# Performance work log

Measured on AMD Instinct MI355X. Metric: run time of the kernel, lower is better.

Reference implementation:

```python
import jax, jax.numpy as jnp
import numpy as np

SHAPES = ((100, 100), (50, 50), (25, 25))  # (H_l, W_l) per level
D, HEADS, HD, L, P = 256, 8, 32, 3, 4


def setup_inputs() -> dict:
    key = jax.random.key(0)
    ks = jax.random.split(key, 12)
    B = 2
    Nq = sum(h * w for h, w in SHAPES)  # 13125
    inp = {
        "query": jax.random.normal(ks[0], (B, Nq, D), jnp.float32),
        "reference_points": jax.random.uniform(ks[1], (B, Nq, L, 2), jnp.float32),
        "value0": jax.random.normal(ks[2], (B, SHAPES[0][0] * SHAPES[0][1], D), jnp.float32),
        "value1": jax.random.normal(ks[3], (B, SHAPES[1][0] * SHAPES[1][1], D), jnp.float32),
        "value2": jax.random.normal(ks[4], (B, SHAPES[2][0] * SHAPES[2][1], D), jnp.float32),
        "W_val": jax.random.normal(ks[5], (D, D), jnp.float32) * 0.05,
        "b_val": jnp.zeros((D,), jnp.float32),
        "W_off": jax.random.normal(ks[6], (D, HEADS * L * P * 2), jnp.float32) * 0.01,
        "b_off": jax.random.normal(ks[7], (HEADS * L * P * 2,), jnp.float32) * 2.0,
        "W_attn": jax.random.normal(ks[8], (D, HEADS * L * P), jnp.float32) * 0.02,
        "b_attn": jnp.zeros((HEADS * L * P,), jnp.float32),
        "W_out": jax.random.normal(ks[9], (D, D), jnp.float32) * 0.05,
        "b_out": jnp.zeros((D,), jnp.float32),
    }
    return inp


def _bilinear_sample(v, Hl, Wl, loc):
    """v: (B, heads, Hl*Wl, hd); loc: (B, Nq, heads, P, 2) normalized coords in [0,1].
    Matches torch F.grid_sample(mode='bilinear', padding_mode='zeros', align_corners=False)
    applied to grid = 2*loc - 1. Returns (B, Nq, heads, P, hd)."""
    B, heads, _, hd = v.shape
    Nq, Pn = loc.shape[1], loc.shape[3]
    # align_corners=False: pixel = ((g+1)*size - 1)/2 with g = 2*loc-1  ->  loc*size - 0.5
    x = loc[..., 0] * Wl - 0.5
    y = loc[..., 1] * Hl - 0.5
    x0 = jnp.floor(x)
    y0 = jnp.floor(y)
    wx1 = x - x0
    wy1 = y - y0
    out = jnp.zeros((B, Nq, heads, Pn, hd), v.dtype)
    for xi, wx in ((x0, 1.0 - wx1), (x0 + 1.0, wx1)):
        for yi, wy in ((y0, 1.0 - wy1), (y0 + 1.0, wy1)):
            inb = (xi >= 0) & (xi < Wl) & (yi >= 0) & (yi < Hl)
            idx = (jnp.clip(yi, 0, Hl - 1) * Wl + jnp.clip(xi, 0, Wl - 1)).astype(jnp.int32)
            idx_t = idx.transpose(0, 2, 1, 3).reshape(B, heads, Nq * Pn)  # (B,H,Nq*P)
            g = jnp.take_along_axis(v, idx_t[..., None], axis=2)  # (B,H,Nq*P,hd)
            g = g.reshape(B, heads, Nq, Pn, hd).transpose(0, 2, 1, 3, 4)
            w = (wx * wy * inb).astype(v.dtype)  # (B,Nq,heads,P)
            out = out + g * w[..., None]
    return out


def _forward(query, reference_points, values, W_val, b_val, W_off, b_off, W_attn, b_attn, W_out, b_out):
    B, Nq, _ = query.shape
    offs = (query @ W_off + b_off).reshape(B, Nq, HEADS, L, P, 2)
    attn = jax.nn.softmax((query @ W_attn + b_attn).reshape(B, Nq, HEADS, L * P), axis=-1)
    attn = attn.reshape(B, Nq, HEADS, L, P)
    out = jnp.zeros((B, Nq, HEADS, HD), query.dtype)
    for lvl, (Hl, Wl) in enumerate(SHAPES):
        # project values, split heads: (B, heads, H*W, hd)
        v = (values[lvl] @ W_val + b_val).reshape(B, Hl * Wl, HEADS, HD).transpose(0, 2, 1, 3)
        norm = jnp.array([Wl, Hl], query.dtype)
        loc = reference_points[:, :, lvl][:, :, None, None, :] + offs[:, :, :, lvl] / norm  # (B,Nq,heads,P,2)
        sampled = _bilinear_sample(v, Hl, Wl, loc)  # (B,Nq,heads,P,hd)
        out = out + jnp.einsum('bnhp,bnhpd->bnhd', attn[:, :, :, lvl], sampled)
    out = out.reshape(B, Nq, D)
    return out @ W_out + b_out  # dropout is identity at eval


def reference(query, reference_points, value0, value1, value2, W_val, b_val, W_off, b_off, W_attn, b_attn, W_out, b_out):
    return _forward(query, reference_points, (value0, value1, value2), W_val, b_val, W_off, b_off, W_attn, b_attn, W_out, b_out)
```

## Files before the change

kernel.cpp:

```cpp
#include <hip/hip_runtime.h>
#include <hip/hip_bf16.h>
#include <math.h>

#define BATCH 2
#define NQ    13125
#define MQ    26250
#define DM    256
#define NH    8
#define HDIM  32
#define NL    3
#define NP    4
#define NTOK  13125

typedef __attribute__((ext_vector_type(8))) short bf16x8;
typedef __attribute__((ext_vector_type(4))) float f32x4;

__device__ __forceinline__ short f2bf(float f) {
    unsigned u = __float_as_uint(f);
    unsigned r = (u + 0x7FFFu + ((u >> 16) & 1u)) >> 16;
    return (short)r;
}
__device__ __forceinline__ float bf2f(unsigned short u) {
    return __uint_as_float((unsigned)u << 16);
}

__global__ __launch_bounds__(256) void wprep_kernel(const float* __restrict__ Wv,
                                                    const float* __restrict__ Wo,
                                                    const float* __restrict__ Wa,
                                                    const float* __restrict__ Wu,
                                                    short* __restrict__ Wt)
{
    const int w = blockIdx.y;
    const int Ns[4]   = {256, 192, 96, 256};
    const int Offs[4] = {0, 256 * 256, 256 * 256 + 192 * 256, 256 * 256 + 192 * 256 + 96 * 256};
    const float* W = (w == 0) ? Wv : ((w == 1) ? Wo : ((w == 2) ? Wa : Wu));
    const int N = Ns[w];
    const int flat = blockIdx.x * 256 + threadIdx.x;
    const int n = flat >> 8, k = flat & 255;
    if (n < N) Wt[Offs[w] + n * 256 + k] = f2bf(W[k * N + n]);
}

__global__ __launch_bounds__(256) void cvt_kernel(const float* __restrict__ q,
                                                  const float* __restrict__ v0,
                                                  const float* __restrict__ v1,
                                                  const float* __restrict__ v2,
                                                  short* __restrict__ qb,
                                                  short* __restrict__ v0b,
                                                  short* __restrict__ v1b,
                                                  short* __restrict__ v2b)
{
    const int t = blockIdx.y;
    const int sz4[4] = {MQ * 64, 2 * 10000 * 64, 2 * 2500 * 64, 2 * 625 * 64};
    const float* src = (t == 0) ? q : ((t == 1) ? v0 : ((t == 2) ? v1 : v2));
    short* dst = (t == 0) ? qb : ((t == 1) ? v0b : ((t == 2) ? v1b : v2b));
    const int i = blockIdx.x * 256 + threadIdx.x;
    if (i < sz4[t]) {
        float4 v = ((const float4*)src)[i];
        short4 o;
        o.x = f2bf(v.x); o.y = f2bf(v.y); o.z = f2bf(v.z); o.w = f2bf(v.w);
        ((short4*)dst)[i] = o;
    }
}

template<int EPI>
__device__ __forceinline__ void gemm_body(const short* __restrict__ A,
                                          const short* __restrict__ Wt,
                                          const float* __restrict__ bias0,
                                          const float* __restrict__ bias1,
                                          void* __restrict__ C0,
                                          void* __restrict__ C1,
                                          int M, int N, int m0, int n0)
{
    __shared__ short As[128][40];
    __shared__ short Bs[64][40];

    const int tid  = threadIdx.x;
    const int lane = tid & 63;
    const int wave = tid >> 6;
    const int wm   = wave * 32;
    const int ml   = lane & 15;
    const int kq   = lane >> 4;

    const int srow = tid >> 2;
    const int skp  = (tid & 3) * 8;

    f32x4 acc[2][4] = {};

    for (int k0 = 0; k0 < 256; k0 += 32) {
#pragma unroll
        for (int rr = 0; rr < 2; ++rr) {
            const int row = srow + rr * 64;
            bf16x8 t = {};
            if (m0 + row < M) t = *(const bf16x8*)(A + (size_t)(m0 + row) * 256 + k0 + skp);
            *(bf16x8*)&As[row][skp] = t;
        }
        {
            bf16x8 t = {};
            if (n0 + srow < N) t = *(const bf16x8*)(Wt + (size_t)(n0 + srow) * 256 + k0 + skp);
            *(bf16x8*)&Bs[srow][skp] = t;
        }
        __syncthreads();

        bf16x8 af[2], bfr[4];
#pragma unroll
        for (int ti = 0; ti < 2; ++ti) af[ti] = *(const bf16x8*)&As[wm + ti * 16 + ml][kq * 8];
#pragma unroll
        for (int tj = 0; tj < 4; ++tj) bfr[tj] = *(const bf16x8*)&Bs[tj * 16 + ml][kq * 8];
#pragma unroll
        for (int ti = 0; ti < 2; ++ti)
#pragma unroll
            for (int tj = 0; tj < 4; ++tj)
                acc[ti][tj] = __builtin_amdgcn_mfma_f32_16x16x32_bf16(af[ti], bfr[tj], acc[ti][tj], 0, 0, 0);

        __syncthreads();
    }

#pragma unroll
    for (int ti = 0; ti < 2; ++ti) {
#pragma unroll
        for (int tj = 0; tj < 4; ++tj) {
#pragma unroll
            for (int r = 0; r < 4; ++r) {
                const int gm = m0 + wm + ti * 16 + kq * 4 + r;
                const int gn = n0 + tj * 16 + ml;
                if (gm >= M || gn >= N) continue;
                if (EPI == 0) {
                    ((float*)C0)[(size_t)gm * N + gn] = acc[ti][tj][r] + bias0[gn];
                } else if (EPI == 1) {
                    ((short*)C0)[(size_t)gm * N + gn] = f2bf(acc[ti][tj][r] + bias0[gn]);
                } else {
                    if (gn < 192) ((float*)C0)[(size_t)gm * 192 + gn] = acc[ti][tj][r] + bias0[gn];
                    else          ((float*)C1)[(size_t)gm * 96 + gn - 192] = acc[ti][tj][r] + bias1[gn - 192];
                }
            }
        }
    }
}

__global__ __launch_bounds__(256) void qgemm_fused_kernel(const short* __restrict__ A,
                                                          const short* __restrict__ Wt,
                                                          const float* __restrict__ b_off,
                                                          const float* __restrict__ b_attn,
                                                          float* __restrict__ offs,
                                                          float* __restrict__ lgts)
{
    const int m0 = blockIdx.y * 128;
    const int n0 = blockIdx.x * 64;
    gemm_body<2>(A, Wt, b_off, b_attn, offs, lgts, MQ, 288, m0, n0);
}

__global__ __launch_bounds__(256) void ogemm_kernel(const short* __restrict__ A,
                                                    const short* __restrict__ Wt,
                                                    const float* __restrict__ bias,
                                                    float* __restrict__ C)
{
    const int m0 = blockIdx.y * 128;
    const int n0 = blockIdx.x * 64;
    gemm_body<0>(A, Wt, bias, nullptr, C, nullptr, MQ, DM, m0, n0);
}

__global__ __launch_bounds__(256) void vproj_kernel(const short* __restrict__ v0b,
                                                    const short* __restrict__ v1b,
                                                    const short* __restrict__ v2b,
                                                    const short* __restrict__ Wt,
                                                    const float* __restrict__ bias,
                                                    short* __restrict__ vws)
{
    const int z = blockIdx.z;
    const int b = z / 3, l = z % 3;
    const int Ms[3]   = {10000, 2500, 625};
    const int Offs[3] = {0, 10000, 12500};
    const short* Asel = (l == 0) ? v0b : ((l == 1) ? v1b : v2b);
    const int M = Ms[l];
    const short* A = Asel + (size_t)b * M * DM;
    short* C = vws + ((size_t)b * NTOK + Offs[l]) * DM;
    const int m0 = blockIdx.y * 128;
    const int n0 = blockIdx.x * 64;
    if (m0 >= M) return;
    gemm_body<1>(A, Wt, bias, nullptr, C, nullptr, M, DM, m0, n0);
}

__global__ __launch_bounds__(256) void sample_kernel(const short* __restrict__ vws,
                                                     const float* __restrict__ offs,
                                                     const float* __restrict__ logits,
                                                     const float* __restrict__ refp,
                                                     short* __restrict__ mid)
{
    const int q0  = blockIdx.x * 4;
    const int tid = threadIdx.x;

    __shared__ float  s_lg[4][96];
    __shared__ float  s_ref[4][6];
    __shared__ float  s_stat[4][NH][2];
    __shared__ float4 s_w[4][96];
    __shared__ int4   s_i[4][96];

    for (int idx = tid; idx < 384; idx += 256) {
        const int qq = idx / 96, s = idx % 96;
        const int q = q0 + qq;
        if (q < MQ) s_lg[qq][s] = logits[(size_t)q * 96 + s];
    }
    if (tid < 24) {
        const int qq = tid / 6, j = tid % 6;
        const int q = q0 + qq;
        if (q < MQ) s_ref[qq][j] = refp[(size_t)q * 6 + j];
    }
    __syncthreads();

    if (tid < 32) {
        const int qq = tid >> 3, h = tid & 7;
        if (q0 + qq < MQ) {
            float mx = -1e30f;
#pragma unroll
            for (int i = 0; i < 12; ++i) mx = fmaxf(mx, s_lg[qq][h * 12 + i]);
            float ssum = 0.f;
#pragma unroll
            for (int i = 0; i < 12; ++i) ssum += expf(s_lg[qq][h * 12 + i] - mx);
            s_stat[qq][h][0] = mx;
            s_stat[qq][h][1] = 1.f / ssum;
        }
    }
    __syncthreads();

    for (int idx = tid; idx < 384; idx += 256) {
        const int qq = idx / 96, s = idx % 96;
        const int q  = q0 + qq;
        if (q >= MQ) continue;
        const int b  = q / NQ;
        const int h  = s / 12, i = s % 12;
        const int l  = i >> 2, p = i & 3;

        const int Hs[3] = {100, 50, 25};
        const int Wz[3] = {100, 50, 25};
        const int Lo[3] = {0, 10000, 12500};
        const int Wl = Wz[l], Hl = Hs[l];
        const float fW = (float)Wl, fH = (float)Hl;

        const float aw = expf(s_lg[qq][s] - s_stat[qq][h][0]) * s_stat[qq][h][1];

        const int oi = (((h * NL) + l) * NP + p) * 2;
        const float2 offp = *(const float2*)(offs + (size_t)q * 192 + oi);
        const float rx = s_ref[qq][l * 2 + 0];
        const float ry = s_ref[qq][l * 2 + 1];

        const float x = (rx + offp.x / fW) * fW - 0.5f;
        const float y = (ry + offp.y / fH) * fH - 0.5f;
        const float x0f = floorf(x), y0f = floorf(y);
        const int   x0 = (int)x0f,  y0 = (int)y0f;
        const float wx1 = x - x0f, wy1 = y - y0f;
        const float wx0 = 1.f - wx1, wy0 = 1.f - wy1;

        const bool xin0 = (x0 >= 0) && (x0 < Wl);
        const bool xin1 = (x0 + 1 >= 0) && (x0 + 1 < Wl);
        const bool yin0 = (y0 >= 0) && (y0 < Hl);
        const bool yin1 = (y0 + 1 >= 0) && (y0 + 1 < Hl);

        const int cx0 = min(max(x0, 0), Wl - 1);
        const int cx1 = min(max(x0 + 1, 0), Wl - 1);
        const int cy0 = min(max(y0, 0), Hl - 1);
        const int cy1 = min(max(y0 + 1, 0), Hl - 1);

        const int base = b * NTOK + Lo[l];
        int4 idxv;
        idxv.x = base + cy0 * Wl + cx0;
        idxv.y = base + cy0 * Wl + cx1;
        idxv.z = base + cy1 * Wl + cx0;
        idxv.w = base + cy1 * Wl + cx1;

        float4 w;
        w.x = (xin0 && yin0) ? aw * wx0 * wy0 : 0.f;
        w.y = (xin1 && yin0) ? aw * wx1 * wy0 : 0.f;
        w.z = (xin0 && yin1) ? aw * wx0 * wy1 : 0.f;
        w.w = (xin1 && yin1) ? aw * wx1 * wy1 : 0.f;

        s_w[qq][s] = w;
        s_i[qq][s] = idxv;
    }
    __syncthreads();

    {
        const int qq = tid >> 6;
        const int q  = q0 + qq;
        if (q < MQ) {
            const int r  = tid & 63;
            const int h  = r >> 3;
            const int c4 = (r & 7) * 4;
            const int ch = h * HDIM + c4;

            float a0 = 0.f, a1 = 0.f, a2 = 0.f, a3 = 0.f;
#pragma unroll
            for (int s = 0; s < 12; ++s) {
                const float4 w  = s_w[qq][h * 12 + s];
                const int4   id = s_i[qq][h * 12 + s];
                const ushort4 u0 = *(const ushort4*)(vws + (size_t)id.x * DM + ch);
                const ushort4 u1 = *(const ushort4*)(vws + (size_t)id.y * DM + ch);
                const ushort4 u2 = *(const ushort4*)(vws + (size_t)id.z * DM + ch);
                const ushort4 u3 = *(const ushort4*)(vws + (size_t)id.w * DM + ch);
                a0 += w.x * bf2f(u0.x) + w.y * bf2f(u1.x) + w.z * bf2f(u2.x) + w.w * bf2f(u3.x);
                a1 += w.x * bf2f(u0.y) + w.y * bf2f(u1.y) + w.z * bf2f(u2.y) + w.w * bf2f(u3.y);
                a2 += w.x * bf2f(u0.z) + w.y * bf2f(u1.z) + w.z * bf2f(u2.z) + w.w * bf2f(u3.z);
                a3 += w.x * bf2f(u0.w) + w.y * bf2f(u1.w) + w.z * bf2f(u2.w) + w.w * bf2f(u3.w);
            }
            short4 o;
            o.x = f2bf(a0); o.y = f2bf(a1); o.z = f2bf(a2); o.w = f2bf(a3);
            *(short4*)(mid + (size_t)q * DM + ch) = o;
        }
    }
}

extern "C" void kernel_launch(void* const* d_in, const int* in_sizes, int n_in,
                              void* d_out, int out_size, void* d_ws, size_t ws_size,
                              hipStream_t stream)
{
    const float* query  = (const float*)d_in[0];
    const float* refp   = (const float*)d_in[1];
    const float* v0     = (const float*)d_in[2];
    const float* v1     = (const float*)d_in[3];
    const float* v2     = (const float*)d_in[4];
    const float* W_val  = (const float*)d_in[5];
    const float* b_val  = (const float*)d_in[6];
    const float* W_off  = (const float*)d_in[7];
    const float* b_off  = (const float*)d_in[8];
    const float* W_attn = (const float*)d_in[9];
    const float* b_attn = (const float*)d_in[10];
    const float* W_out  = (const float*)d_in[11];
    const float* b_out  = (const float*)d_in[12];
    float* out = (float*)d_out;

    float* ws   = (float*)d_ws;
    float* offs = ws;
    float* lgts = offs + (size_t)MQ * 192;
    short* vws  = (short*)(lgts + (size_t)MQ * 96);
    short* mid  = vws + (size_t)BATCH * NTOK * DM;
    short* qbf  = mid + (size_t)MQ * DM;
    short* v0b  = qbf + (size_t)MQ * DM;
    short* v1b  = v0b + (size_t)2 * 10000 * DM;
    short* v2b  = v1b + (size_t)2 * 2500 * DM;
    short* Wt   = v2b + (size_t)2 * 625 * DM;
    short* Wt_val  = Wt;
    short* Wt_off  = Wt_val + 256 * 256;
    short* Wt_out  = Wt_off + 288 * 256;

    {
        dim3 grid(256, 4);
        wprep_kernel<<<grid, 256, 0, stream>>>(W_val, W_off, W_attn, W_out, Wt);
    }
    {
        dim3 grid((MQ * 64 + 255) / 256, 4);
        cvt_kernel<<<grid, 256, 0, stream>>>(query, v0, v1, v2, qbf, v0b, v1b, v2b);
    }
    {
        dim3 grid(DM / 64, (10000 + 127) / 128, 6);
        vproj_kernel<<<grid, 256, 0, stream>>>(v0b, v1b, v2b, Wt_val, b_val, vws);
    }
    {
        dim3 grid((288 + 63) / 64, (MQ + 127) / 128);
        qgemm_fused_kernel<<<grid, 256, 0, stream>>>(qbf, Wt_off, b_off, b_attn, offs, lgts);
    }
    sample_kernel<<<(MQ + 3) / 4, 256, 0, stream>>>(vws, offs, lgts, refp, mid);
    {
        dim3 grid(DM / 64, (MQ + 127) / 128);
        ogemm_kernel<<<grid, 256, 0, stream>>>(mid, Wt_out, b_out, out);
    }
}
```

Measured before the change: 240.9 us.

## Use 128x128 GEMM tiles with direct global-to-LDS loads and widen sampling gathers

Replaces the 128x64 GEMM with a 128x128 tile kernel. It loads A and B straight into LDS via global_load_lds and uses an XOR-swizzled LDS layout to avoid bank conflicts. Value tensors are converted into one concatenated buffer so the value projection becomes a single GEMM launch, and the offset/attention weight matrix is zero-padded to 384 columns. The sampling kernel moves to 128 threads with 8-wide bf16 gathers and byte offsets precomputed in the index table. Larger tiles cut redundant operand loads and launches, but lower block count, occupancy and padding waste are risks.

```diff
diff --git a/kernel.cpp b/kernel.cpp
--- a/kernel.cpp
+++ b/kernel.cpp
@@ -13,6 +13,7 @@
 #define NTOK  13125
 
 typedef __attribute__((ext_vector_type(8))) short bf16x8;
+typedef __attribute__((ext_vector_type(8))) unsigned short u16x8;
 typedef __attribute__((ext_vector_type(4))) float f32x4;
 
 __device__ __forceinline__ short f2bf(float f) {
@@ -22,6 +23,12 @@
 }
 __device__ __forceinline__ float bf2f(unsigned short u) {
     return __uint_as_float((unsigned)u << 16);
+}
+
+__device__ __forceinline__ void gld_lds16(const short* g, short* l) {
+    __builtin_amdgcn_global_load_lds(
+        (const __attribute__((address_space(1))) unsigned int*)g,
+        (__attribute__((address_space(3))) unsigned int*)l, 16, 0, 0);
 }
 
 __global__ __launch_bounds__(256) void wprep_kernel(const float* __restrict__ Wv,
@@ -31,13 +38,15 @@
                                                     short* __restrict__ Wt)
 {
     const int w = blockIdx.y;
-    const int Ns[4]   = {256, 192, 96, 256};
-    const int Offs[4] = {0, 256 * 256, 256 * 256 + 192 * 256, 256 * 256 + 192 * 256 + 96 * 256};
-    const float* W = (w == 0) ? Wv : ((w == 1) ? Wo : ((w == 2) ? Wa : Wu));
+    const int Ns[5]   = {256, 192, 96, 256, 96};
+    const int Offs[5] = {0, 65536, 114688, 163840, 139264};
     const int N = Ns[w];
     const int flat = blockIdx.x * 256 + threadIdx.x;
     const int n = flat >> 8, k = flat & 255;
-    if (n < N) Wt[Offs[w] + n * 256 + k] = f2bf(W[k * N + n]);
+    if (n >= N) return;
+    if (w == 4) { Wt[139264 + n * 256 + k] = 0; return; }
+    const float* W = (w == 0) ? Wv : ((w == 1) ? Wo : ((w == 2) ? Wa : Wu));
+    Wt[Offs[w] + n * 256 + k] = f2bf(W[k * N + n]);
 }
 
 __global__ __launch_bounds__(256) void cvt_kernel(const float* __restrict__ q,
@@ -45,69 +54,83 @@
                                                   const float* __restrict__ v1,
                                                   const float* __restrict__ v2,
                                                   short* __restrict__ qb,
-                                                  short* __restrict__ v0b,
-                                                  short* __restrict__ v1b,
-                                                  short* __restrict__ v2b)
+                                                  short* __restrict__ vcat)
 {
     const int t = blockIdx.y;
     const int sz4[4] = {MQ * 64, 2 * 10000 * 64, 2 * 2500 * 64, 2 * 625 * 64};
+    const int i = blockIdx.x * 256 + threadIdx.x;
+    if (i >= sz4[t]) return;
+    const int row = i >> 6, c = i & 63;
     const float* src = (t == 0) ? q : ((t == 1) ? v0 : ((t == 2) ? v1 : v2));
-    short* dst = (t == 0) ? qb : ((t == 1) ? v0b : ((t == 2) ? v1b : v2b));
-    const int i = blockIdx.x * 256 + threadIdx.x;
-    if (i < sz4[t]) {
-        float4 v = ((const float4*)src)[i];
-        short4 o;
-        o.x = f2bf(v.x); o.y = f2bf(v.y); o.z = f2bf(v.z); o.w = f2bf(v.w);
-        ((short4*)dst)[i] = o;
-    }
-}
-
-template<int EPI>
-__device__ __forceinline__ void gemm_body(const short* __restrict__ A,
-                                          const short* __restrict__ Wt,
-                                          const float* __restrict__ bias0,
-                                          const float* __restrict__ bias1,
-                                          void* __restrict__ C0,
-                                          void* __restrict__ C1,
-                                          int M, int N, int m0, int n0)
-{
-    __shared__ short As[128][40];
-    __shared__ short Bs[64][40];
+    int orow;
+    short* dst;
+    if (t == 0)      { orow = row;                                        dst = qb; }
+    else if (t == 1) { orow = (row / 10000) * NTOK + (row % 10000);       dst = vcat; }
+    else if (t == 2) { orow = (row / 2500) * NTOK + 10000 + (row % 2500); dst = vcat; }
+    else             { orow = (row / 625) * NTOK + 12500 + (row % 625);   dst = vcat; }
+    float4 v = ((const float4*)src)[i];
+    short4 o;
+    o.x = f2bf(v.x); o.y = f2bf(v.y); o.z = f2bf(v.z); o.w = f2bf(v.w);
+    ((short4*)dst)[orow * 64 + c] = o;
+}
+
+template<int EPI, int NN>
+__global__ __launch_bounds__(256) void gemm128(const short* __restrict__ A,
+                                               const short* __restrict__ Wt,
+                                               const float* __restrict__ bias0,
+                                               const float* __restrict__ bias1,
+                                               void* __restrict__ C0,
+                                               void* __restrict__ C1)
+{
+    __shared__ short As[128 * 32];
+    __shared__ short Bs[128 * 32];
 
     const int tid  = threadIdx.x;
+    const int m0   = blockIdx.y * 128;
+    const int n0   = blockIdx.x * 128;
     const int lane = tid & 63;
     const int wave = tid >> 6;
-    const int wm   = wave * 32;
+    const int wm   = (wave & 1) * 64;
+    const int wn   = (wave >> 1) * 64;
     const int ml   = lane & 15;
     const int kq   = lane >> 4;
 
-    const int srow = tid >> 2;
-    const int skp  = (tid & 3) * 8;
-
-    f32x4 acc[2][4] = {};
+    const int row0 = tid >> 2;
+    const int row1 = row0 + 64;
+    const int kqs  = (tid & 3) ^ ((row0 >> 1) & 3);
+    const short* gA0 = A  + (size_t)(m0 + row0) * 256 + kqs * 8;
+    const short* gA1 = A  + (size_t)(m0 + row1) * 256 + kqs * 8;
+    const short* gB0 = Wt + (size_t)(n0 + row0) * 256 + kqs * 8;
+    const short* gB1 = Wt + (size_t)(n0 + row1) * 256 + kqs * 8;
+    short* lA0 = As + tid * 8;
+    short* lA1 = As + (256 + tid) * 8;
+    short* lB0 = Bs + tid * 8;
+    short* lB1 = Bs + (256 + tid) * 8;
+    const bool a0ok = (m0 + row0) < MQ;
+    const bool a1ok = (m0 + row1) < MQ;
+
+    f32x4 acc[4][4] = {};
 
     for (int k0 = 0; k0 < 256; k0 += 32) {
-#pragma unroll
-        for (int rr = 0; rr < 2; ++rr) {
-            const int row = srow + rr * 64;
-            bf16x8 t = {};
-            if (m0 + row < M) t = *(const bf16x8*)(A + (size_t)(m0 + row) * 256 + k0 + skp);
-            *(bf16x8*)&As[row][skp] = t;
-        }
-        {
-            bf16x8 t = {};
-            if (n0 + srow < N) t = *(const bf16x8*)(Wt + (size_t)(n0 + srow) * 256 + k0 + skp);
-            *(bf16x8*)&Bs[srow][skp] = t;
-        }
+        if (a0ok) gld_lds16(gA0 + k0, lA0);
+        if (a1ok) gld_lds16(gA1 + k0, lA1);
+        gld_lds16(gB0 + k0, lB0);
+        gld_lds16(gB1 + k0, lB1);
         __syncthreads();
 
-        bf16x8 af[2], bfr[4];
-#pragma unroll
-        for (int ti = 0; ti < 2; ++ti) af[ti] = *(const bf16x8*)&As[wm + ti * 16 + ml][kq * 8];
-#pragma unroll
-        for (int tj = 0; tj < 4; ++tj) bfr[tj] = *(const bf16x8*)&Bs[tj * 16 + ml][kq * 8];
-#pragma unroll
-        for (int ti = 0; ti < 2; ++ti)
+        bf16x8 af[4], bfr[4];
+#pragma unroll
+        for (int ti = 0; ti < 4; ++ti) {
+            const int r = wm + ti * 16 + ml;
+            af[ti] = *(const bf16x8*)&As[r * 32 + ((kq ^ ((r >> 1) & 3)) << 3)];
+        }
+#pragma unroll
+        for (int tj = 0; tj < 4; ++tj) {
+            const int r = wn + tj * 16 + ml;
+            bfr[tj] = *(const bf16x8*)&Bs[r * 32 + ((kq ^ ((r >> 1) & 3)) << 3)];
+        }
+#pragma unroll
+        for (int ti = 0; ti < 4; ++ti)
 #pragma unroll
             for (int tj = 0; tj < 4; ++tj)
                 acc[ti][tj] = __builtin_amdgcn_mfma_f32_16x16x32_bf16(af[ti], bfr[tj], acc[ti][tj], 0, 0, 0);
@@ -116,71 +139,29 @@
     }
 
 #pragma unroll
-    for (int ti = 0; ti < 2; ++ti) {
-#pragma unroll
-        for (int tj = 0; tj < 4; ++tj) {
+    for (int tj = 0; tj < 4; ++tj) {
+        const int gn = n0 + wn + tj * 16 + ml;
+#pragma unroll
+        for (int ti = 0; ti < 4; ++ti) {
 #pragma unroll
             for (int r = 0; r < 4; ++r) {
                 const int gm = m0 + wm + ti * 16 + kq * 4 + r;
-                const int gn = n0 + tj * 16 + ml;
-                if (gm >= M || gn >= N) continue;
+                if (gm >= MQ) continue;
+                const float v = acc[ti][tj][r];
                 if (EPI == 0) {
-                    ((float*)C0)[(size_t)gm * N + gn] = acc[ti][tj][r] + bias0[gn];
+                    ((float*)C0)[(size_t)gm * NN + gn] = v + bias0[gn];
                 } else if (EPI == 1) {
-                    ((short*)C0)[(size_t)gm * N + gn] = f2bf(acc[ti][tj][r] + bias0[gn]);
+                    ((short*)C0)[(size_t)gm * NN + gn] = f2bf(v + bias0[gn]);
                 } else {
-                    if (gn < 192) ((float*)C0)[(size_t)gm * 192 + gn] = acc[ti][tj][r] + bias0[gn];
-                    else          ((float*)C1)[(size_t)gm * 96 + gn - 192] = acc[ti][tj][r] + bias1[gn - 192];
+                    if (gn < 192)      ((float*)C0)[(size_t)gm * 192 + gn]        = v + bias0[gn];
+                    else if (gn < 288) ((float*)C1)[(size_t)gm * 96 + (gn - 192)] = v + bias1[gn - 192];
                 }
             }
         }
     }
 }
 
-__global__ __launch_bounds__(256) void qgemm_fused_kernel(const short* __restrict__ A,
-                                                          const short* __restrict__ Wt,
-                                                          const float* __restrict__ b_off,
-                                                          const float* __restrict__ b_attn,
-                                                          float* __restrict__ offs,
-                                                          float* __restrict__ lgts)
-{
-    const int m0 = blockIdx.y * 128;
-    const int n0 = blockIdx.x * 64;
-    gemm_body<2>(A, Wt, b_off, b_attn, offs, lgts, MQ, 288, m0, n0);
-}
-
-__global__ __launch_bounds__(256) void ogemm_kernel(const short* __restrict__ A,
-                                                    const short* __restrict__ Wt,
-                                                    const float* __restrict__ bias,
-                                                    float* __restrict__ C)
-{
-    const int m0 = blockIdx.y * 128;
-    const int n0 = blockIdx.x * 64;
-    gemm_body<0>(A, Wt, bias, nullptr, C, nullptr, MQ, DM, m0, n0);
-}
-
-__global__ __launch_bounds__(256) void vproj_kernel(const short* __restrict__ v0b,
-                                                    const short* __restrict__ v1b,
-                                                    const short* __restrict__ v2b,
-                                                    const short* __restrict__ Wt,
-                                                    const float* __restrict__ bias,
-                                                    short* __restrict__ vws)
-{
-    const int z = blockIdx.z;
-    const int b = z / 3, l = z % 3;
-    const int Ms[3]   = {10000, 2500, 625};
-    const int Offs[3] = {0, 10000, 12500};
-    const short* Asel = (l == 0) ? v0b : ((l == 1) ? v1b : v2b);
-    const int M = Ms[l];
-    const short* A = Asel + (size_t)b * M * DM;
-    short* C = vws + ((size_t)b * NTOK + Offs[l]) * DM;
-    const int m0 = blockIdx.y * 128;
-    const int n0 = blockIdx.x * 64;
-    if (m0 >= M) return;
-    gemm_body<1>(A, Wt, bias, nullptr, C, nullptr, M, DM, m0, n0);
-}
-
-__global__ __launch_bounds__(256) void sample_kernel(const short* __restrict__ vws,
+__global__ __launch_bounds__(128) void sample_kernel(const short* __restrict__ vws,
                                                      const float* __restrict__ offs,
                                                      const float* __restrict__ logits,
                                                      const float* __restrict__ refp,
@@ -195,15 +176,13 @@
     __shared__ float4 s_w[4][96];
     __shared__ int4   s_i[4][96];
 
-    for (int idx = tid; idx < 384; idx += 256) {
+    for (int idx = tid; idx < 384; idx += 128) {
         const int qq = idx / 96, s = idx % 96;
-        const int q = q0 + qq;
-        if (q < MQ) s_lg[qq][s] = logits[(size_t)q * 96 + s];
+        if (q0 + qq < MQ) s_lg[qq][s] = logits[(size_t)(q0 + qq) * 96 + s];
     }
     if (tid < 24) {
         const int qq = tid / 6, j = tid % 6;
-        const int q = q0 + qq;
-        if (q < MQ) s_ref[qq][j] = refp[(size_t)q * 6 + j];
+        if (q0 + qq < MQ) s_ref[qq][j] = refp[(size_t)(q0 + qq) * 6 + j];
     }
     __syncthreads();
 
@@ -222,7 +201,7 @@
     }
     __syncthreads();
 
-    for (int idx = tid; idx < 384; idx += 256) {
+    for (int idx = tid; idx < 384; idx += 128) {
         const int qq = idx / 96, s = idx % 96;
         const int q  = q0 + qq;
         if (q >= MQ) continue;
@@ -262,10 +241,10 @@
 
         const int base = b * NTOK + Lo[l];
         int4 idxv;
-        idxv.x = base + cy0 * Wl + cx0;
-        idxv.y = base + cy0 * Wl + cx1;
-        idxv.z = base + cy1 * Wl + cx0;
-        idxv.w = base + cy1 * Wl + cx1;
+        idxv.x = (base + cy0 * Wl + cx0) * 512;
+        idxv.y = (base + cy0 * Wl + cx1) * 512;
+        idxv.z = (base + cy1 * Wl + cx0) * 512;
+        idxv.w = (base + cy1 * Wl + cx1) * 512;
 
         float4 w;
         w.x = (xin0 && yin0) ? aw * wx0 * wy0 : 0.f;
@@ -279,31 +258,32 @@
     __syncthreads();
 
     {
-        const int qq = tid >> 6;
+        const int qq = tid >> 5;
         const int q  = q0 + qq;
         if (q < MQ) {
-            const int r  = tid & 63;
-            const int h  = r >> 3;
-            const int c4 = (r & 7) * 4;
-            const int ch = h * HDIM + c4;
-
-            float a0 = 0.f, a1 = 0.f, a2 = 0.f, a3 = 0.f;
+            const int r  = tid & 31;
+            const int h  = r >> 2;
+            const int c8 = (r & 3) * 8;
+            const int ch = h * HDIM + c8;
+            const char* vb = (const char*)vws + (size_t)ch * 2;
+
+            float a[8] = {};
 #pragma unroll
             for (int s = 0; s < 12; ++s) {
                 const float4 w  = s_w[qq][h * 12 + s];
                 const int4   id = s_i[qq][h * 12 + s];
-                const ushort4 u0 = *(const ushort4*)(vws + (size_t)id.x * DM + ch);
-                const ushort4 u1 = *(const ushort4*)(vws + (size_t)id.y * DM + ch);
-                const ushort4 u2 = *(const ushort4*)(vws + (size_t)id.z * DM + ch);
-                const ushort4 u3 = *(const ushort4*)(vws + (size_t)id.w * DM + ch);
-                a0 += w.x * bf2f(u0.x) + w.y * bf2f(u1.x) + w.z * bf2f(u2.x) + w.w * bf2f(u3.x);
-                a1 += w.x * bf2f(u0.y) + w.y * bf2f(u1.y) + w.z * bf2f(u2.y) + w.w * bf2f(u3.y);
-                a2 += w.x * bf2f(u0.z) + w.y * bf2f(u1.z) + w.z * bf2f(u2.z) + w.w * bf2f(u3.z);
-                a3 += w.x * bf2f(u0.w) + w.y * bf2f(u1.w) + w.z * bf2f(u2.w) + w.w * bf2f(u3.w);
+                const u16x8 u0 = *(const u16x8*)(vb + id.x);
+                const u16x8 u1 = *(const u16x8*)(vb + id.y);
+                const u16x8 u2 = *(const u16x8*)(vb + id.z);
+                const u16x8 u3 = *(const u16x8*)(vb + id.w);
+#pragma unroll
+                for (int j = 0; j < 8; ++j)
+                    a[j] += w.x * bf2f(u0[j]) + w.y * bf2f(u1[j]) + w.z * bf2f(u2[j]) + w.w * bf2f(u3[j]);
             }
-            short4 o;
-            o.x = f2bf(a0); o.y = f2bf(a1); o.z = f2bf(a2); o.w = f2bf(a3);
-            *(short4*)(mid + (size_t)q * DM + ch) = o;
+            union { u16x8 v; unsigned short s[8]; } o;
+#pragma unroll
+            for (int j = 0; j < 8; ++j) o.s[j] = (unsigned short)f2bf(a[j]);
+            *(u16x8*)(mid + (size_t)q * DM + ch) = o.v;
         }
     }
 }
@@ -331,35 +311,33 @@
     float* offs = ws;
     float* lgts = offs + (size_t)MQ * 192;
     short* vws  = (short*)(lgts + (size_t)MQ * 96);
-    short* mid  = vws + (size_t)BATCH * NTOK * DM;
+    short* mid  = vws + (size_t)MQ * DM;
     short* qbf  = mid + (size_t)MQ * DM;
-    short* v0b  = qbf + (size_t)MQ * DM;
-    short* v1b  = v0b + (size_t)2 * 10000 * DM;
-    short* v2b  = v1b + (size_t)2 * 2500 * DM;
-    short* Wt   = v2b + (size_t)2 * 625 * DM;
-    short* Wt_val  = Wt;
-    short* Wt_off  = Wt_val + 256 * 256;
-    short* Wt_out  = Wt_off + 288 * 256;
-
-    {
-        dim3 grid(256, 4);
+    short* vcat = qbf + (size_t)MQ * DM;
+    short* Wt   = vcat + (size_t)MQ * DM;
+    short* Wt_val = Wt;
+    short* Wt_off = Wt + 65536;
+    short* Wt_out = Wt + 163840;
+
+    {
+        dim3 grid(256, 5);
         wprep_kernel<<<grid, 256, 0, stream>>>(W_val, W_off, W_attn, W_out, Wt);
     }
     {
         dim3 grid((MQ * 64 + 255) / 256, 4);
-        cvt_kernel<<<grid, 256, 0, stream>>>(query, v0, v1, v2, qbf, v0b, v1b, v2b);
-    }
-    {
-        dim3 grid(DM / 64, (10000 + 127) / 128, 6);
-        vproj_kernel<<<grid, 256, 0, stream>>>(v0b, v1b, v2b, Wt_val, b_val, vws);
-    }
-    {
-        dim3 grid((288 + 63) / 64, (MQ + 127) / 128);
-        qgemm_fused_kernel<<<grid, 256, 0, stream>>>(qbf, Wt_off, b_off, b_attn, offs, lgts);
-    }
-    sample_kernel<<<(MQ + 3) / 4, 256, 0, stream>>>(vws, offs, lgts, refp, mid);
-    {
-        dim3 grid(DM / 64, (MQ + 127) / 128);
-        ogemm_kernel<<<grid, 256, 0, stream>>>(mid, Wt_out, b_out, out);
-    }
-}
+        cvt_kernel<<<grid, 256, 0, stream>>>(query, v0, v1, v2, qbf, vcat);
+    }
+    {
+        dim3 grid(2, (MQ + 127) / 128);
+        gemm128<1, 256><<<grid, 256, 0, stream>>>(vcat, Wt_val, b_val, nullptr, vws, nullptr);
+    }
+    {
+        dim3 grid(3, (MQ + 127) / 128);
+        gemm128<2, 384><<<grid, 256, 0, stream>>>(qbf, Wt_off, b_off, b_attn, offs, lgts);
+    }
+    sample_kernel<<<(MQ + 3) / 4, 128, 0, stream>>>(vws, offs, lgts, refp, mid);
+    {
+        dim3 grid(2, (MQ + 127) / 128);
+        gemm128<0, 256><<<grid, 256, 0, stream>>>(mid, Wt_out, b_out, nullptr, out, nullptr);
+    }
+}
```

Result: no change. 240.4 us (-0.2%).
